# Performance work log

Measured on AMD Instinct MI355X. Metric: run time of the kernel, lower is better.

Reference implementation:

```python
import jax, jax.numpy as jnp
import numpy as np

K = 100  # number of negative samples
EPS = 1e-6


def setup_inputs() -> dict:
    key = jax.random.key(0)
    k1, k2, k3 = jax.random.split(key, 3)
    B, V = 1024, 100000
    noise_logits = jax.random.normal(k1, (B, V), dtype=jnp.float32)
    actual_logits = jax.random.normal(k2, (B, K + 1), dtype=jnp.float32)
    target_id = jax.random.randint(k3, (B,), 0, V, dtype=jnp.int64)
    return {"noise_logits": noise_logits, "actual_logits": actual_logits, "target_id": target_id}


def reference(noise_logits, actual_logits, target_id):
    B, V = noise_logits.shape
    # Mask the target item out (torch: one_hot scatter then softmax*one_hot, renormalized
    # implicitly by multinomial). Equivalent: set target logit to -inf.
    neg_inf = jnp.finfo(noise_logits.dtype).min
    masked = noise_logits.at[jnp.arange(B), target_id].set(neg_inf)
    # Without-replacement multinomial from softmax(masked) via Gumbel top-k.
    g = jax.random.gumbel(jax.random.key(42), (B, V), dtype=noise_logits.dtype)
    _, neg_items = jax.lax.top_k(masked + g, K)  # [B, K]
    pos_neg_items = jnp.concatenate([target_id[:, None].astype(neg_items.dtype), neg_items], axis=1)  # [B, K+1]
    # Scoring
    noise_prob = jnp.take_along_axis(noise_logits, pos_neg_items, axis=1)  # [B, K+1]
    noise_prob = jax.nn.softmax(noise_prob, axis=-1)
    actual_prob = jax.nn.softmax(actual_logits, axis=-1)
    deno = K * noise_prob + actual_prob + EPS
    tmp1 = actual_prob / deno
    tmp2 = noise_prob / deno
    likeli = jnp.concatenate([tmp1[:, :1], tmp2[:, 1:]], axis=1)
    likeli = jnp.where(likeli == 1.0, 1.0 + EPS, likeli)
    return -jnp.mean(jnp.log(likeli))
```

## Files before the change

### kernel.cpp

```cpp
#include <hip/hip_runtime.h>
#include <stdint.h>

#define NROWS   1024
#define NV      100000
#define NSEL    101
#define NBINS   2048
#define POOLSZ  3072
#define NTHR    512
#define CHUNK   2048
#define NCHUNK  ((NV + CHUNK - 1) / CHUNK)

__device__ __forceinline__ uint32_t rotl32(uint32_t x, uint32_t r) {
  return (x << r) | (x >> (32u - r));
}

__device__ __forceinline__ uint32_t jax_random_bits(uint32_t n) {
  const uint32_t K1 = 42u;
  const uint32_t K2 = 0x1BD11BF0u;
  uint32_t x0 = 0u;
  uint32_t x1 = n + K1;
#define TF_R(r) { x0 += x1; x1 = rotl32(x1, (r)); x1 ^= x0; }
  TF_R(13u) TF_R(15u) TF_R(26u) TF_R(6u)
  x0 += K1; x1 += K2 + 1u;
  TF_R(17u) TF_R(29u) TF_R(16u) TF_R(24u)
  x0 += K2; x1 += 0u + 2u;
  TF_R(13u) TF_R(15u) TF_R(26u) TF_R(6u)
  x0 += 0u; x1 += K1 + 3u;
  TF_R(17u) TF_R(29u) TF_R(16u) TF_R(24u)
  x0 += K1; x1 += K2 + 4u;
  TF_R(13u) TF_R(15u) TF_R(26u) TF_R(6u)
  x0 += K2; x1 += 0u + 5u;
#undef TF_R
  return x0 ^ x1;
}

__device__ __forceinline__ float jax_gumbel(uint32_t n) {
  uint32_t bits = jax_random_bits(n);
  float f = __uint_as_float((bits >> 9) | 0x3f800000u) - 1.0f;
  f = fmaxf(f, 1.1754943508222875e-38f);
  return -__logf(-__logf(f));
}

__device__ __forceinline__ float blk_reduce(float x, int tid, float* wred, bool is_max) {
  #pragma unroll
  for (int off = 32; off >= 1; off >>= 1) {
    float o = __shfl_down(x, off);
    x = is_max ? fmaxf(x, o) : (x + o);
  }
  if ((tid & 63) == 0) wred[tid >> 6] = x;
  __syncthreads();
  float r = wred[0];
  #pragma unroll
  for (int w = 1; w < NTHR / 64; ++w)
    r = is_max ? fmaxf(r, wred[w]) : (r + wred[w]);
  __syncthreads();
  return r;
}

__device__ __forceinline__ uint32_t sortable_bin(float v) {
  uint32_t fb = __float_as_uint(v);
  uint32_t key = fb ^ (uint32_t)(((int32_t)fb >> 31) | (int32_t)0x80000000);
  return key >> 21;
}

__global__ void __launch_bounds__(NTHR, 8)
nce_row_kernel(const float* __restrict__ noise, const float* __restrict__ actual,
               const int* __restrict__ target, float* __restrict__ acc,
               uint32_t* __restrict__ ticket, float* __restrict__ out) {
  const int row = blockIdx.x;
  const int tid = threadIdx.x;
  const int lane = tid & 63;

  __shared__ float    pv[POOLSZ];
  __shared__ uint32_t pi[POOLSZ];
  __shared__ uint32_t hist[NBINS];
  __shared__ uint32_t s_cnt;
  __shared__ uint32_t s_thr;
  __shared__ float    s_wred[NTHR / 64];

  for (int i = tid; i < NBINS; i += NTHR) hist[i] = 0u;
  if (tid == 0) { s_cnt = 0u; s_thr = 0u; }
  __syncthreads();

  const float* rowp = noise + (size_t)row * NV;
  const uint32_t tgt = (uint32_t)target[row];
  const uint32_t nbase = (uint32_t)row * (uint32_t)NV;

  float4 a;
  {
    const int v0 = tid * 4;
    if (v0 < NV) a = *reinterpret_cast<const float4*>(rowp + v0);
  }

  for (int c = 0; c < NCHUNK; ++c) {
    float4 a_next;
    {
      const int vn = (c + 1) * CHUNK + tid * 4;
      if (c + 1 < NCHUNK && vn < NV)
        a_next = *reinterpret_cast<const float4*>(rowp + vn);
    }

    const uint32_t thr = s_thr;
    const int v = c * CHUNK + tid * 4;
    const float av[4] = {a.x, a.y, a.z, a.w};
    #pragma unroll
    for (int j = 0; j < 4; ++j) {
      const uint32_t col = (uint32_t)(v + j);
      const bool valid = (v + j) < NV;
      const float logit = (col == tgt) ? -3.4028234663852886e+38f : av[j];
      const float val = logit + jax_gumbel(nbase + col);
      const uint32_t bin = sortable_bin(val);
      const bool pred = valid && (bin >= thr);
      const unsigned long long mask = __ballot(pred);
      if (mask) {
        const int leader = __ffsll((long long)mask) - 1;
        uint32_t base = 0;
        if (lane == leader) base = atomicAdd(&s_cnt, (uint32_t)__popcll(mask));
        base = __shfl(base, leader);
        if (pred) {
          const uint32_t pos = base + (uint32_t)__popcll(mask & ((1ull << lane) - 1ull));
          if (pos < POOLSZ) { pv[pos] = val; pi[pos] = col; }
          atomicAdd(&hist[bin], 1u);
        }
      }
    }
    __syncthreads();

    if (tid < 64) {
      const int bpl = NBINS / 64;
      uint32_t sum = 0;
      const uint32_t base = (uint32_t)tid * bpl;
      #pragma unroll
      for (int j = 0; j < bpl; ++j) sum += hist[base + j];
      uint32_t suf = sum;
      #pragma unroll
      for (int off = 1; off < 64; off <<= 1) {
        uint32_t o = __shfl_down(suf, off);
        if (tid + off < 64) suf += o;
      }
      const uint32_t sufnext = suf - sum;
      if (suf >= 100u && sufnext < 100u) {
        uint32_t cum = sufnext;
        uint32_t b = base + bpl - 1;
        for (;; --b) { cum += hist[b]; if (cum >= 100u) break; }
        if (b > s_thr) s_thr = b;
      }
    }
    __syncthreads();

    if (s_cnt > (uint32_t)(POOLSZ - CHUNK)) {
      const uint32_t n = min(s_cnt, (uint32_t)POOLSZ);
      const uint32_t thr2 = s_thr;
      float lv[POOLSZ / NTHR]; uint32_t li[POOLSZ / NTHR]; int nkeep = 0;
      for (uint32_t p = tid; p < n; p += NTHR) {
        float val = pv[p];
        if (sortable_bin(val) >= thr2) { lv[nkeep] = val; li[nkeep] = pi[p]; ++nkeep; }
      }
      __syncthreads();
      if (tid == 0) s_cnt = 0u;
      __syncthreads();
      for (int k = 0; k < nkeep; ++k) {
        uint32_t pos = atomicAdd(&s_cnt, 1u);
        if (pos < POOLSZ) { pv[pos] = lv[k]; pi[pos] = li[k]; }
      }
      __syncthreads();
    }
    a = a_next;
  }
  __syncthreads();

  const uint32_t n = min(s_cnt, (uint32_t)2048);
  uint32_t sortn = 128;
  while (sortn < n) sortn <<= 1;
  for (uint32_t i = n + tid; i < sortn; i += NTHR) { pv[i] = -INFINITY; pi[i] = 0xFFFFFFFFu; }
  __syncthreads();

  for (uint32_t ksz = 2; ksz <= sortn; ksz <<= 1) {
    for (uint32_t jsz = ksz >> 1; jsz >= 1; jsz >>= 1) {
      for (uint32_t i = tid; i < sortn; i += NTHR) {
        const uint32_t ixj = i ^ jsz;
        if (ixj > i) {
          const bool desc = ((i & ksz) == 0);
          float va = pv[i], vb = pv[ixj];
          uint32_t ia = pi[i], ib = pi[ixj];
          const bool a_less = (va < vb) || (va == vb && ia > ib);
          if (desc ? a_less : !a_less) {
            pv[i] = vb; pv[ixj] = va; pi[i] = ib; pi[ixj] = ia;
          }
        }
      }
      __syncthreads();
    }
  }

  float nl = -INFINITY, al = -INFINITY;
  if (tid < NSEL) {
    const uint32_t idx = (tid == 0) ? tgt : pi[tid - 1];
    nl = rowp[idx];
    al = actual[(size_t)row * NSEL + tid];
  }
  const float mn = blk_reduce(nl, tid, s_wred, true);
  const float ma = blk_reduce(al, tid, s_wred, true);
  const float en = (tid < NSEL) ? __expf(nl - mn) : 0.0f;
  const float ea = (tid < NSEL) ? __expf(al - ma) : 0.0f;
  const float sn = blk_reduce(en, tid, s_wred, false);
  const float sa = blk_reduce(ea, tid, s_wred, false);

  float contrib = 0.0f;
  if (tid < NSEL) {
    const float npj = en / sn;
    const float apj = ea / sa;
    const float deno = 100.0f * npj + apj + 1e-6f;
    float t = (tid == 0) ? (apj / deno) : (npj / deno);
    if (t == 1.0f) t = 1.0f + 1e-6f;
    contrib = logf(t);
  }
  const float tot = blk_reduce(contrib, tid, s_wred, false);

  if (tid == 0) {
    atomicAdd(acc, tot);
    __threadfence();
    const uint32_t t = atomicAdd(ticket, 1u);
    if (t == (uint32_t)(NROWS - 1)) {
      const float total = atomicAdd(acc, 0.0f) + 0.0f;
      out[0] = -total / (1024.0f * 101.0f);
    }
  }
}

extern "C" void kernel_launch(void* const* d_in, const int* in_sizes, int n_in,
                              void* d_out, int out_size, void* d_ws, size_t ws_size,
                              hipStream_t stream) {
  const float* noise  = (const float*)d_in[0];
  const float* actual = (const float*)d_in[1];
  const int*   target = (const int*)d_in[2];
  float* out = (float*)d_out;
  float*    acc    = (float*)d_ws;
  uint32_t* ticket = (uint32_t*)d_ws + 1;

  hipMemsetAsync(d_ws, 0, 8, stream);
  nce_row_kernel<<<NROWS, NTHR, 0, stream>>>(noise, actual, target, acc, ticket, out);
}
```

Before: 807.6 us.

## Split row into per-wave stripes with private pools and cheap Gumbel pre-filter

Each of the 8 waves now scans its own contiguous 12500-element stripe and keeps a private candidate pool. This removes the per-chunk block-wide syncthreads and the shared pool-counter atomics. A cheap bound on the Gumbel value, taken from the leading-zero count of the random mantissa, lets whole wavefronts skip the two logs when no lane can pass the current threshold. The threshold is raised asynchronously through a shared atomicMax, and the pools are merged and filtered at the end before one fixed 1024-element bitonic sort. The risks are the correctness of the clz-based bound, dropped candidates if a wave pool overflows, and handling of the target column, which is now excluded only at merge time.

```diff
diff --git a/kernel.cpp b/kernel.cpp
--- a/kernel.cpp
+++ b/kernel.cpp
@@ -4,11 +4,12 @@
 #define NROWS   1024
 #define NV      100000
 #define NSEL    101
-#define NBINS   2048
-#define POOLSZ  3072
+#define NEED    101
+#define POOLW   480
+#define NWAVE   8
 #define NTHR    512
-#define CHUNK   2048
-#define NCHUNK  ((NV + CHUNK - 1) / CHUNK)
+#define STRIPE  12500
+#define FULLIT  48
 
 __device__ __forceinline__ uint32_t rotl32(uint32_t x, uint32_t r) {
   return (x << r) | (x >> (32u - r));
@@ -34,13 +35,6 @@
   return x0 ^ x1;
 }
 
-__device__ __forceinline__ float jax_gumbel(uint32_t n) {
-  uint32_t bits = jax_random_bits(n);
-  float f = __uint_as_float((bits >> 9) | 0x3f800000u) - 1.0f;
-  f = fmaxf(f, 1.1754943508222875e-38f);
-  return -__logf(-__logf(f));
-}
-
 __device__ __forceinline__ float blk_reduce(float x, int tid, float* wred, bool is_max) {
   #pragma unroll
   for (int off = 32; off >= 1; off >>= 1) {
@@ -57,10 +51,81 @@
   return r;
 }
 
-__device__ __forceinline__ uint32_t sortable_bin(float v) {
-  uint32_t fb = __float_as_uint(v);
-  uint32_t key = fb ^ (uint32_t)(((int32_t)fb >> 31) | (int32_t)0x80000000);
-  return key >> 21;
+__device__ __forceinline__ uint32_t hist_phys(uint32_t b) {
+  return ((b & 31u) << 6) | (b >> 5);
+}
+
+__device__ __forceinline__ float binlow_float(uint32_t b) {
+  uint32_t k = b << 21;
+  if (k & 0x80000000u) {
+    uint32_t fb = k ^ 0x80000000u;
+    return (fb >= 0x7F800000u) ? INFINITY : __uint_as_float(fb);
+  } else {
+    uint32_t fb = ~k;
+    return (fb >= 0xFF800000u) ? -INFINITY : __uint_as_float(fb);
+  }
+}
+
+__device__ __forceinline__ int wave_scan_thr(volatile uint32_t* hist, int lane, uint32_t need) {
+  uint32_t sum = 0;
+  #pragma unroll
+  for (int j = 0; j < 32; ++j) sum += hist[(j << 6) | lane];
+  uint32_t suf = sum;
+  #pragma unroll
+  for (int off = 1; off < 64; off <<= 1) {
+    uint32_t o = __shfl_down(suf, off);
+    if (lane + off < 64) suf += o;
+  }
+  const uint32_t sufnext = suf - sum;
+  int b = -1;
+  if (suf >= need && sufnext < need) {
+    uint32_t cum = sufnext;
+    int j = 31;
+    for (;; --j) {
+      cum += hist[(j << 6) | lane];
+      if (cum >= need || j == 0) break;
+    }
+    b = lane * 32 + j;
+  }
+  #pragma unroll
+  for (int off = 32; off >= 1; off >>= 1) b = max(b, __shfl_xor(b, off));
+  return b;
+}
+
+__device__ __forceinline__ void raise_thr(int b, int lane, uint32_t* thrkey, volatile float* thrf) {
+  if (b < 0) return;
+  if (lane == 0) {
+    uint32_t old = atomicMax(thrkey, (uint32_t)b);
+    if ((uint32_t)b > old) *thrf = binlow_float((uint32_t)b);
+  }
+}
+
+__device__ __forceinline__ void proc_elem(
+    float logit, uint32_t n, uint32_t col, float thrf, float thr_s, int lane,
+    float* pv_w, uint32_t* pi_w, uint32_t* hist, uint32_t& cnt) {
+  const uint32_t bits = jax_random_bits(n);
+  const uint32_t b23 = bits >> 9;
+  const uint32_t m = 0x800000u - b23;
+  const float clzf = (float)__clz((int)m);
+  const float req = fmaf(logit, -1.4426950408889634f, thr_s);
+  const bool maybe = (clzf >= req);
+  if (__ballot(maybe) == 0ull) return;
+  float f1 = __uint_as_float(b23 | 0x3f800000u) - 1.0f;
+  float u = fmaxf(f1, 1.1754943508222875e-38f);
+  const float g = -__logf(-__logf(u));
+  const float val = logit + g;
+  const bool pred = maybe && (val >= thrf);
+  const unsigned long long mk = __ballot(pred);
+  if (mk == 0ull) return;
+  const uint32_t pos = cnt + (uint32_t)__popcll(mk & ((1ull << lane) - 1ull));
+  if (pred && pos < (uint32_t)POOLW) {
+    pv_w[pos] = val;
+    pi_w[pos] = col;
+    uint32_t fb = __float_as_uint(val);
+    uint32_t key = fb ^ (uint32_t)(((int32_t)fb >> 31) | (int32_t)0x80000000);
+    atomicAdd(&hist[hist_phys(key >> 21)], 1u);
+  }
+  cnt += (uint32_t)__popcll(mk);
 }
 
 __global__ void __launch_bounds__(NTHR, 8)
@@ -70,122 +135,139 @@
   const int row = blockIdx.x;
   const int tid = threadIdx.x;
   const int lane = tid & 63;
-
-  __shared__ float    pv[POOLSZ];
-  __shared__ uint32_t pi[POOLSZ];
-  __shared__ uint32_t hist[NBINS];
-  __shared__ uint32_t s_cnt;
-  __shared__ uint32_t s_thr;
+  const uint32_t w = (uint32_t)tid >> 6;
+
+  __shared__ float    pv[NWAVE * POOLW];
+  __shared__ uint32_t pi_[NWAVE * POOLW];
+  __shared__ uint32_t uni[2048];
+  __shared__ uint32_t s_cnt[NWAVE];
+  __shared__ uint32_t s_thrkey;
+  __shared__ float    s_thrf;
+  __shared__ float    s_thrf_final;
+  __shared__ uint32_t s_mcnt;
   __shared__ float    s_wred[NTHR / 64];
 
-  for (int i = tid; i < NBINS; i += NTHR) hist[i] = 0u;
-  if (tid == 0) { s_cnt = 0u; s_thr = 0u; }
+  uint32_t* hist = uni;
+  float*    mv   = (float*)uni;
+  uint32_t* mi   = uni + 1024;
+
+  for (int i = tid; i < 2048; i += NTHR) hist[i] = 0u;
+  if (tid == 0) { s_thrkey = 0u; s_thrf = -INFINITY; s_mcnt = 0u; }
   __syncthreads();
 
   const float* rowp = noise + (size_t)row * NV;
   const uint32_t tgt = (uint32_t)target[row];
   const uint32_t nbase = (uint32_t)row * (uint32_t)NV;
-
-  float4 a;
+  const uint32_t stripe0 = w * (uint32_t)STRIPE;
+  const float* sp = rowp + stripe0;
+  float*    pv_w = pv  + w * POOLW;
+  uint32_t* pi_w = pi_ + w * POOLW;
+  volatile float* vthrf = &s_thrf;
+
+  uint32_t cnt = 0;
+  const float qnan = __int_as_float(0x7fc00000);
+
+  float4 a = *reinterpret_cast<const float4*>(sp + lane * 4);
+
+  for (int it = 0; it < FULLIT; ++it) {
+    float4 an;
+    if (it < FULLIT - 1) {
+      an = *reinterpret_cast<const float4*>(sp + (it + 1) * 256 + lane * 4);
+    } else if (lane < 53) {
+      an = *reinterpret_cast<const float4*>(sp + FULLIT * 256 + lane * 4);
+    }
+
+    const float thrf = *vthrf;
+    const float thr_s = fmaf(thrf, 1.4426950408889634f, 8.0f);
+    const uint32_t e0 = stripe0 + (uint32_t)(it * 256 + lane * 4);
+    proc_elem(a.x, nbase + e0 + 0u, e0 + 0u, thrf, thr_s, lane, pv_w, pi_w, hist, cnt);
+    proc_elem(a.y, nbase + e0 + 1u, e0 + 1u, thrf, thr_s, lane, pv_w, pi_w, hist, cnt);
+    proc_elem(a.z, nbase + e0 + 2u, e0 + 2u, thrf, thr_s, lane, pv_w, pi_w, hist, cnt);
+    proc_elem(a.w, nbase + e0 + 3u, e0 + 3u, thrf, thr_s, lane, pv_w, pi_w, hist, cnt);
+
+    if (cnt > (uint32_t)(POOLW - 256)) {
+      int b = wave_scan_thr(hist, lane, NEED);
+      raise_thr(b, lane, &s_thrkey, vthrf);
+      const float tf = *vthrf;
+      const uint32_t n0 = min(cnt, (uint32_t)POOLW);
+      uint32_t nc = 0;
+      for (uint32_t p0 = 0; p0 < n0; p0 += 64) {
+        const uint32_t p = p0 + (uint32_t)lane;
+        const bool v = (p < n0);
+        float vv = 0.0f; uint32_t ii = 0;
+        if (v) { vv = pv_w[p]; ii = pi_w[p]; }
+        const bool keep = v && (vv >= tf);
+        const unsigned long long km = __ballot(keep);
+        const uint32_t np = nc + (uint32_t)__popcll(km & ((1ull << lane) - 1ull));
+        if (keep) { pv_w[np] = vv; pi_w[np] = ii; }
+        nc += (uint32_t)__popcll(km);
+      }
+      cnt = nc;
+    } else if ((it & 15) == 7) {
+      int b = wave_scan_thr(hist, lane, NEED);
+      raise_thr(b, lane, &s_thrkey, vthrf);
+    }
+    a = an;
+  }
+
   {
-    const int v0 = tid * 4;
-    if (v0 < NV) a = *reinterpret_cast<const float4*>(rowp + v0);
-  }
-
-  for (int c = 0; c < NCHUNK; ++c) {
-    float4 a_next;
-    {
-      const int vn = (c + 1) * CHUNK + tid * 4;
-      if (c + 1 < NCHUNK && vn < NV)
-        a_next = *reinterpret_cast<const float4*>(rowp + vn);
-    }
-
-    const uint32_t thr = s_thr;
-    const int v = c * CHUNK + tid * 4;
-    const float av[4] = {a.x, a.y, a.z, a.w};
-    #pragma unroll
-    for (int j = 0; j < 4; ++j) {
-      const uint32_t col = (uint32_t)(v + j);
-      const bool valid = (v + j) < NV;
-      const float logit = (col == tgt) ? -3.4028234663852886e+38f : av[j];
-      const float val = logit + jax_gumbel(nbase + col);
-      const uint32_t bin = sortable_bin(val);
-      const bool pred = valid && (bin >= thr);
-      const unsigned long long mask = __ballot(pred);
-      if (mask) {
-        const int leader = __ffsll((long long)mask) - 1;
-        uint32_t base = 0;
-        if (lane == leader) base = atomicAdd(&s_cnt, (uint32_t)__popcll(mask));
-        base = __shfl(base, leader);
-        if (pred) {
-          const uint32_t pos = base + (uint32_t)__popcll(mask & ((1ull << lane) - 1ull));
-          if (pos < POOLSZ) { pv[pos] = val; pi[pos] = col; }
-          atomicAdd(&hist[bin], 1u);
-        }
+    const float thrf = *vthrf;
+    const float thr_s = fmaf(thrf, 1.4426950408889634f, 8.0f);
+    const uint32_t e0 = stripe0 + (uint32_t)(FULLIT * 256 + lane * 4);
+    const bool lv = (lane < 53);
+    proc_elem(lv ? a.x : qnan, nbase + e0 + 0u, e0 + 0u, thrf, thr_s, lane, pv_w, pi_w, hist, cnt);
+    proc_elem(lv ? a.y : qnan, nbase + e0 + 1u, e0 + 1u, thrf, thr_s, lane, pv_w, pi_w, hist, cnt);
+    proc_elem(lv ? a.z : qnan, nbase + e0 + 2u, e0 + 2u, thrf, thr_s, lane, pv_w, pi_w, hist, cnt);
+    proc_elem(lv ? a.w : qnan, nbase + e0 + 3u, e0 + 3u, thrf, thr_s, lane, pv_w, pi_w, hist, cnt);
+  }
+
+  if (lane == 0) s_cnt[w] = min(cnt, (uint32_t)POOLW);
+  __syncthreads();
+
+  if (tid < 64) {
+    int b = wave_scan_thr(hist, lane, NEED);
+    if (lane == 0) s_thrf_final = binlow_float((uint32_t)(b < 0 ? 0 : b));
+  }
+  __syncthreads();
+  const float tf = s_thrf_final;
+
+  for (uint32_t s = tid; s < (uint32_t)(NWAVE * POOLW); s += NTHR) {
+    const uint32_t wq = s / POOLW;
+    const uint32_t p = s - wq * POOLW;
+    bool keep = (p < s_cnt[wq]);
+    float vv = 0.0f; uint32_t ii = 0;
+    if (keep) {
+      vv = pv[s]; ii = pi_[s];
+      keep = (vv >= tf) && (ii != tgt);
+    }
+    const unsigned long long km = __ballot(keep);
+    const uint32_t nb = (uint32_t)__popcll(km);
+    if (nb) {
+      uint32_t base = 0;
+      if (lane == 0) base = atomicAdd(&s_mcnt, nb);
+      base = __shfl(base, 0);
+      if (keep) {
+        const uint32_t pos = base + (uint32_t)__popcll(km & ((1ull << lane) - 1ull));
+        if (pos < 1024u) { mv[pos] = vv; mi[pos] = ii; }
       }
     }
-    __syncthreads();
-
-    if (tid < 64) {
-      const int bpl = NBINS / 64;
-      uint32_t sum = 0;
-      const uint32_t base = (uint32_t)tid * bpl;
-      #pragma unroll
-      for (int j = 0; j < bpl; ++j) sum += hist[base + j];
-      uint32_t suf = sum;
-      #pragma unroll
-      for (int off = 1; off < 64; off <<= 1) {
-        uint32_t o = __shfl_down(suf, off);
-        if (tid + off < 64) suf += o;
-      }
-      const uint32_t sufnext = suf - sum;
-      if (suf >= 100u && sufnext < 100u) {
-        uint32_t cum = sufnext;
-        uint32_t b = base + bpl - 1;
-        for (;; --b) { cum += hist[b]; if (cum >= 100u) break; }
-        if (b > s_thr) s_thr = b;
-      }
-    }
-    __syncthreads();
-
-    if (s_cnt > (uint32_t)(POOLSZ - CHUNK)) {
-      const uint32_t n = min(s_cnt, (uint32_t)POOLSZ);
-      const uint32_t thr2 = s_thr;
-      float lv[POOLSZ / NTHR]; uint32_t li[POOLSZ / NTHR]; int nkeep = 0;
-      for (uint32_t p = tid; p < n; p += NTHR) {
-        float val = pv[p];
-        if (sortable_bin(val) >= thr2) { lv[nkeep] = val; li[nkeep] = pi[p]; ++nkeep; }
-      }
-      __syncthreads();
-      if (tid == 0) s_cnt = 0u;
-      __syncthreads();
-      for (int k = 0; k < nkeep; ++k) {
-        uint32_t pos = atomicAdd(&s_cnt, 1u);
-        if (pos < POOLSZ) { pv[pos] = lv[k]; pi[pos] = li[k]; }
-      }
-      __syncthreads();
-    }
-    a = a_next;
-  }
-  __syncthreads();
-
-  const uint32_t n = min(s_cnt, (uint32_t)2048);
-  uint32_t sortn = 128;
-  while (sortn < n) sortn <<= 1;
-  for (uint32_t i = n + tid; i < sortn; i += NTHR) { pv[i] = -INFINITY; pi[i] = 0xFFFFFFFFu; }
-  __syncthreads();
-
-  for (uint32_t ksz = 2; ksz <= sortn; ksz <<= 1) {
+  }
+  __syncthreads();
+  const uint32_t mc = min(s_mcnt, 1024u);
+  for (uint32_t i = mc + tid; i < 1024u; i += NTHR) { mv[i] = -INFINITY; mi[i] = 0xFFFFFFFFu; }
+  __syncthreads();
+
+  for (uint32_t ksz = 2; ksz <= 1024u; ksz <<= 1) {
     for (uint32_t jsz = ksz >> 1; jsz >= 1; jsz >>= 1) {
-      for (uint32_t i = tid; i < sortn; i += NTHR) {
+      for (uint32_t i = tid; i < 1024u; i += NTHR) {
         const uint32_t ixj = i ^ jsz;
         if (ixj > i) {
           const bool desc = ((i & ksz) == 0);
-          float va = pv[i], vb = pv[ixj];
-          uint32_t ia = pi[i], ib = pi[ixj];
+          float va = mv[i], vb = mv[ixj];
+          uint32_t ia = mi[i], ib = mi[ixj];
           const bool a_less = (va < vb) || (va == vb && ia > ib);
           if (desc ? a_less : !a_less) {
-            pv[i] = vb; pv[ixj] = va; pi[i] = ib; pi[ixj] = ia;
+            mv[i] = vb; mv[ixj] = va; mi[i] = ib; mi[ixj] = ia;
           }
         }
       }
@@ -195,7 +277,7 @@
 
   float nl = -INFINITY, al = -INFINITY;
   if (tid < NSEL) {
-    const uint32_t idx = (tid == 0) ? tgt : pi[tid - 1];
+    const uint32_t idx = (tid == 0) ? tgt : mi[tid - 1];
     nl = rowp[idx];
     al = actual[(size_t)row * NSEL + tid];
   }
@@ -220,9 +302,9 @@
   if (tid == 0) {
     atomicAdd(acc, tot);
     __threadfence();
-    const uint32_t t = atomicAdd(ticket, 1u);
-    if (t == (uint32_t)(NROWS - 1)) {
-      const float total = atomicAdd(acc, 0.0f) + 0.0f;
+    const uint32_t tk = atomicAdd(ticket, 1u);
+    if (tk == (uint32_t)(NROWS - 1)) {
+      const float total = atomicAdd(acc, 0.0f);
       out[0] = -total / (1024.0f * 101.0f);
     }
   }
```

New measurement: 773.0 us. 4.3% less time.
